# Kernel tuning notes

Measured on AMD Instinct MI355X. Metric: run time of the kernel, lower is better.

The kernel has to match this reference:

```python
import jax, jax.numpy as jnp
import numpy as np

N = 8192

def setup_inputs() -> dict:
    key = jax.random.key(0)
    adj = jax.random.uniform(key, (N, N), dtype=jnp.float32)
    return {"adj": adj}

def reference(adj) -> jnp.ndarray:
    # Symmetrize: adj + adj_T*(adj_T>adj) - adj*(adj_T>adj) == elementwise max(adj, adj_T)
    a = jnp.maximum(adj, adj.T)
    # Add self-loops
    a = a + jnp.eye(a.shape[0], dtype=a.dtype)
    # Degree normalization: D^-1/2 A D^-1/2 (diag matmuls == broadcast row/col scaling)
    rowsum = jnp.sum(a, axis=1)
    d_inv_sqrt = jnp.power(rowsum, -0.5)
    d_inv_sqrt = jnp.where(jnp.isinf(d_inv_sqrt), 0.0, d_inv_sqrt)
    return d_inv_sqrt[:, None] * a * d_inv_sqrt[None, :]
```

## Files before the change

kernel.cpp:

```cpp
#include <hip/hip_runtime.h>
#include <math.h>

#define NMAT 8192
#define GT   128
#define NPAIRS (GT * (GT + 1) / 2)

typedef float f4 __attribute__((ext_vector_type(4)));

__device__ __align__(16) float g_part[GT][NMAT];
__device__ __align__(16) float g_dvec[NMAT];

__device__ __forceinline__ int tri_off(int b) {
    return b * GT - ((b * (b - 1)) >> 1);
}

__device__ __forceinline__ void decode_pair(int p, int& bi, int& bj) {
    double dp = (double)p;
    double t = 2.0 * GT + 1.0;
    int b = (int)((t - sqrt(t * t - 8.0 * dp)) * 0.5);
    if (b < 0) b = 0;
    if (b > GT - 1) b = GT - 1;
    while (b + 1 < GT && tri_off(b + 1) <= p) ++b;
    while (b > 0 && tri_off(b) > p) --b;
    bi = b;
    bj = b + (p - tri_off(b));
}

__global__ __launch_bounds__(256) void calc_d() {
    int i = blockIdx.x * blockDim.x + threadIdx.x;
    if (i < NMAT) {
        float s = 1.0f;
        #pragma unroll 8
        for (int c = 0; c < GT; ++c) s += g_part[c][i];
        g_dvec[i] = (s > 0.0f) ? (float)(1.0 / sqrt((double)s)) : 0.0f;
    }
}

__global__ __launch_bounds__(256) void pass1_rowsum(const float* __restrict__ A) {
    __shared__ float Yl[64][65];
    __shared__ float colbuf[4][64];

    int bi, bj;
    decode_pair((int)blockIdx.x, bi, bj);

    const int tid   = threadIdx.x;
    const int l16   = tid & 15;
    const int g16   = tid >> 4;
    const int cbase = l16 * 4;
    const int lane  = tid & 63;
    const int w     = tid >> 6;

    const float* Ybase = A + (size_t)(bj * 64) * NMAT + bi * 64;
    const float* Xbase = A + (size_t)(bi * 64) * NMAT + bj * 64;

    f4 y[4], x[4];
    for (int k = 0; k < 4; ++k) {
        int q = k * 16 + g16;
        y[k] = *(const f4*)(Ybase + (size_t)q * NMAT + cbase);
    }
    for (int k = 0; k < 4; ++k) {
        int r = k * 16 + g16;
        x[k] = *(const f4*)(Xbase + (size_t)r * NMAT + cbase);
    }

    for (int k = 0; k < 4; ++k) {
        int q = k * 16 + g16;
        Yl[q][cbase + 0] = y[k].x;
        Yl[q][cbase + 1] = y[k].y;
        Yl[q][cbase + 2] = y[k].z;
        Yl[q][cbase + 3] = y[k].w;
    }
    __syncthreads();

    float cs0 = 0.f, cs1 = 0.f, cs2 = 0.f, cs3 = 0.f;

    for (int k = 0; k < 4; ++k) {
        int r = k * 16 + g16;
        float m0 = fmaxf(x[k].x, Yl[cbase + 0][r]);
        float m1 = fmaxf(x[k].y, Yl[cbase + 1][r]);
        float m2 = fmaxf(x[k].z, Yl[cbase + 2][r]);
        float m3 = fmaxf(x[k].w, Yl[cbase + 3][r]);
        cs0 += m0; cs1 += m1; cs2 += m2; cs3 += m3;
        float rt = (m0 + m1) + (m2 + m3);
        rt += __shfl_xor(rt, 1);
        rt += __shfl_xor(rt, 2);
        rt += __shfl_xor(rt, 4);
        rt += __shfl_xor(rt, 8);
        if (l16 == 0) g_part[bj][bi * 64 + r] = rt;
    }

    if (bi != bj) {
        cs0 += __shfl_xor(cs0, 16); cs0 += __shfl_xor(cs0, 32);
        cs1 += __shfl_xor(cs1, 16); cs1 += __shfl_xor(cs1, 32);
        cs2 += __shfl_xor(cs2, 16); cs2 += __shfl_xor(cs2, 32);
        cs3 += __shfl_xor(cs3, 16); cs3 += __shfl_xor(cs3, 32);
        if (lane < 16) {
            colbuf[w][lane * 4 + 0] = cs0;
            colbuf[w][lane * 4 + 1] = cs1;
            colbuf[w][lane * 4 + 2] = cs2;
            colbuf[w][lane * 4 + 3] = cs3;
        }
        __syncthreads();
        if (tid < 64) {
            float t = (colbuf[0][tid] + colbuf[1][tid]) +
                      (colbuf[2][tid] + colbuf[3][tid]);
            g_part[bi][bj * 64 + tid] = t;
        }
    }
}

__global__ __launch_bounds__(256) void pass2_scale(const float* __restrict__ A,
                                                   float* __restrict__ out) {
    __shared__ float Yl[64][65];

    int bi, bj;
    decode_pair(NPAIRS - 1 - (int)blockIdx.x, bi, bj);

    const int tid   = threadIdx.x;
    const int l16   = tid & 15;
    const int g16   = tid >> 4;
    const int cbase = l16 * 4;

    const float* Ybase = A + (size_t)(bj * 64) * NMAT + bi * 64;
    const float* Xbase = A + (size_t)(bi * 64) * NMAT + bj * 64;

    f4 y[4], x[4];
    for (int k = 0; k < 4; ++k) {
        int q = k * 16 + g16;
        y[k] = *(const f4*)(Ybase + (size_t)q * NMAT + cbase);
    }
    for (int k = 0; k < 4; ++k) {
        int r = k * 16 + g16;
        x[k] = *(const f4*)(Xbase + (size_t)r * NMAT + cbase);
    }

    for (int k = 0; k < 4; ++k) {
        int q = k * 16 + g16;
        Yl[q][cbase + 0] = y[k].x;
        Yl[q][cbase + 1] = y[k].y;
        Yl[q][cbase + 2] = y[k].z;
        Yl[q][cbase + 3] = y[k].w;
    }
    __syncthreads();

    const f4 dj = *(const f4*)(g_dvec + bj * 64 + cbase);
    const bool diag = (bi == bj);

    for (int k = 0; k < 4; ++k) {
        int r = k * 16 + g16;
        float di = g_dvec[bi * 64 + r];
        float m0 = fmaxf(x[k].x, Yl[cbase + 0][r]);
        float m1 = fmaxf(x[k].y, Yl[cbase + 1][r]);
        float m2 = fmaxf(x[k].z, Yl[cbase + 2][r]);
        float m3 = fmaxf(x[k].w, Yl[cbase + 3][r]);
        if (diag) {
            if (r == cbase + 0) m0 += 1.0f;
            if (r == cbase + 1) m1 += 1.0f;
            if (r == cbase + 2) m2 += 1.0f;
            if (r == cbase + 3) m3 += 1.0f;
        }
        f4 v;
        v.x = di * dj.x * m0;
        v.y = di * dj.y * m1;
        v.z = di * dj.z * m2;
        v.w = di * dj.w * m3;
        __builtin_nontemporal_store(v, (f4*)(out + (size_t)(bi * 64 + r) * NMAT + bj * 64 + cbase));
        Yl[cbase + 0][r] = v.x;
        Yl[cbase + 1][r] = v.y;
        Yl[cbase + 2][r] = v.z;
        Yl[cbase + 3][r] = v.w;
    }

    if (!diag) {
        __syncthreads();
        for (int k = 0; k < 4; ++k) {
            int q = k * 16 + g16;
            f4 v;
            v.x = Yl[q][cbase + 0];
            v.y = Yl[q][cbase + 1];
            v.z = Yl[q][cbase + 2];
            v.w = Yl[q][cbase + 3];
            __builtin_nontemporal_store(v, (f4*)(out + (size_t)(bj * 64 + q) * NMAT + bi * 64 + cbase));
        }
    }
}

extern "C" void kernel_launch(void* const* d_in, const int* in_sizes, int n_in,
                              void* d_out, int out_size, void* d_ws, size_t ws_size,
                              hipStream_t stream) {
    const float* A = (const float*)d_in[0];
    float* out     = (float*)d_out;

    pass1_rowsum<<<NPAIRS, 256, 0, stream>>>(A);
    calc_d<<<NMAT / 256, 256, 0, stream>>>();
    pass2_scale<<<NPAIRS, 256, 0, stream>>>(A, out);
}
```

Measured before the change: 489.4 us.

## Enlarge transpose tiles to 128x128 with XOR-swizzled shared memory

Doubles the symmetric tile size from 64 to 128, using 1024-thread blocks and half as many tile-row partials. Shared-memory bank conflicts are avoided with an XOR swizzle of the column index instead of padding. Diagonal tiles reuse the already-loaded block instead of loading the transposed copy a second time. Larger blocks with 64KB of shared memory each may limit how many blocks fit per CU and reduce latency hiding.

New measurement: 469.9 us. -4.0%, faster.

```diff
diff --git a/kernel.cpp b/kernel.cpp
--- a/kernel.cpp
+++ b/kernel.cpp
@@ -2,7 +2,8 @@
 #include <math.h>
 
 #define NMAT 8192
-#define GT   128
+#define TS   128
+#define GT   (NMAT / TS)
 #define NPAIRS (GT * (GT + 1) / 2)
 
 typedef float f4 __attribute__((ext_vector_type(4)));
@@ -36,123 +37,135 @@
     }
 }
 
-__global__ __launch_bounds__(256) void pass1_rowsum(const float* __restrict__ A) {
-    __shared__ float Yl[64][65];
-    __shared__ float colbuf[4][64];
+__global__ __launch_bounds__(1024) void pass1_rowsum(const float* __restrict__ A) {
+    __shared__ float Yl[TS][TS];
+    __shared__ float colbuf[16][TS];
 
     int bi, bj;
     decode_pair((int)blockIdx.x, bi, bj);
 
     const int tid   = threadIdx.x;
-    const int l16   = tid & 15;
-    const int g16   = tid >> 4;
-    const int cbase = l16 * 4;
-    const int lane  = tid & 63;
+    const int l32   = tid & 31;
+    const int g32   = tid >> 5;
+    const int cbase = l32 * 4;
     const int w     = tid >> 6;
-
-    const float* Ybase = A + (size_t)(bj * 64) * NMAT + bi * 64;
-    const float* Xbase = A + (size_t)(bi * 64) * NMAT + bj * 64;
-
-    f4 y[4], x[4];
-    for (int k = 0; k < 4; ++k) {
-        int q = k * 16 + g16;
-        y[k] = *(const f4*)(Ybase + (size_t)q * NMAT + cbase);
-    }
-    for (int k = 0; k < 4; ++k) {
-        int r = k * 16 + g16;
-        x[k] = *(const f4*)(Xbase + (size_t)r * NMAT + cbase);
-    }
-
-    for (int k = 0; k < 4; ++k) {
-        int q = k * 16 + g16;
-        Yl[q][cbase + 0] = y[k].x;
-        Yl[q][cbase + 1] = y[k].y;
-        Yl[q][cbase + 2] = y[k].z;
-        Yl[q][cbase + 3] = y[k].w;
+    const bool diag = (bi == bj);
+
+    const float* Xbase = A + (size_t)(bi * TS) * NMAT + bj * TS;
+    const float* Ybase = A + (size_t)(bj * TS) * NMAT + bi * TS;
+
+    f4 x[4], y[4];
+    #pragma unroll
+    for (int k = 0; k < 4; ++k)
+        x[k] = *(const f4*)(Xbase + (size_t)(k * 32 + g32) * NMAT + cbase);
+    if (!diag) {
+        #pragma unroll
+        for (int k = 0; k < 4; ++k)
+            y[k] = *(const f4*)(Ybase + (size_t)(k * 32 + g32) * NMAT + cbase);
+    }
+
+    #pragma unroll
+    for (int k = 0; k < 4; ++k) {
+        int r = k * 32 + g32;
+        f4 v = diag ? x[k] : y[k];
+        int s = (r >> 2) & 31;
+        Yl[r][(cbase + 0) ^ s] = v.x;
+        Yl[r][(cbase + 1) ^ s] = v.y;
+        Yl[r][(cbase + 2) ^ s] = v.z;
+        Yl[r][(cbase + 3) ^ s] = v.w;
     }
     __syncthreads();
 
     float cs0 = 0.f, cs1 = 0.f, cs2 = 0.f, cs3 = 0.f;
 
-    for (int k = 0; k < 4; ++k) {
-        int r = k * 16 + g16;
-        float m0 = fmaxf(x[k].x, Yl[cbase + 0][r]);
-        float m1 = fmaxf(x[k].y, Yl[cbase + 1][r]);
-        float m2 = fmaxf(x[k].z, Yl[cbase + 2][r]);
-        float m3 = fmaxf(x[k].w, Yl[cbase + 3][r]);
+    #pragma unroll
+    for (int k = 0; k < 4; ++k) {
+        int r  = k * 32 + g32;
+        int rs = r ^ l32;
+        float m0 = fmaxf(x[k].x, Yl[cbase + 0][rs]);
+        float m1 = fmaxf(x[k].y, Yl[cbase + 1][rs]);
+        float m2 = fmaxf(x[k].z, Yl[cbase + 2][rs]);
+        float m3 = fmaxf(x[k].w, Yl[cbase + 3][rs]);
         cs0 += m0; cs1 += m1; cs2 += m2; cs3 += m3;
         float rt = (m0 + m1) + (m2 + m3);
         rt += __shfl_xor(rt, 1);
         rt += __shfl_xor(rt, 2);
         rt += __shfl_xor(rt, 4);
         rt += __shfl_xor(rt, 8);
-        if (l16 == 0) g_part[bj][bi * 64 + r] = rt;
-    }
-
-    if (bi != bj) {
-        cs0 += __shfl_xor(cs0, 16); cs0 += __shfl_xor(cs0, 32);
-        cs1 += __shfl_xor(cs1, 16); cs1 += __shfl_xor(cs1, 32);
-        cs2 += __shfl_xor(cs2, 16); cs2 += __shfl_xor(cs2, 32);
-        cs3 += __shfl_xor(cs3, 16); cs3 += __shfl_xor(cs3, 32);
-        if (lane < 16) {
-            colbuf[w][lane * 4 + 0] = cs0;
-            colbuf[w][lane * 4 + 1] = cs1;
-            colbuf[w][lane * 4 + 2] = cs2;
-            colbuf[w][lane * 4 + 3] = cs3;
+        rt += __shfl_xor(rt, 16);
+        if (l32 == 0) g_part[bj][bi * TS + r] = rt;
+    }
+
+    if (!diag) {
+        cs0 += __shfl_xor(cs0, 32);
+        cs1 += __shfl_xor(cs1, 32);
+        cs2 += __shfl_xor(cs2, 32);
+        cs3 += __shfl_xor(cs3, 32);
+        if (!(tid & 32)) {
+            colbuf[w][cbase + 0] = cs0;
+            colbuf[w][cbase + 1] = cs1;
+            colbuf[w][cbase + 2] = cs2;
+            colbuf[w][cbase + 3] = cs3;
         }
         __syncthreads();
-        if (tid < 64) {
-            float t = (colbuf[0][tid] + colbuf[1][tid]) +
-                      (colbuf[2][tid] + colbuf[3][tid]);
-            g_part[bi][bj * 64 + tid] = t;
-        }
-    }
-}
-
-__global__ __launch_bounds__(256) void pass2_scale(const float* __restrict__ A,
-                                                   float* __restrict__ out) {
-    __shared__ float Yl[64][65];
+        if (tid < TS) {
+            float t = 0.f;
+            #pragma unroll
+            for (int v = 0; v < 16; ++v) t += colbuf[v][tid];
+            g_part[bi][bj * TS + tid] = t;
+        }
+    }
+}
+
+__global__ __launch_bounds__(1024) void pass2_scale(const float* __restrict__ A,
+                                                    float* __restrict__ out) {
+    __shared__ float Yl[TS][TS];
 
     int bi, bj;
     decode_pair(NPAIRS - 1 - (int)blockIdx.x, bi, bj);
 
     const int tid   = threadIdx.x;
-    const int l16   = tid & 15;
-    const int g16   = tid >> 4;
-    const int cbase = l16 * 4;
-
-    const float* Ybase = A + (size_t)(bj * 64) * NMAT + bi * 64;
-    const float* Xbase = A + (size_t)(bi * 64) * NMAT + bj * 64;
-
-    f4 y[4], x[4];
-    for (int k = 0; k < 4; ++k) {
-        int q = k * 16 + g16;
-        y[k] = *(const f4*)(Ybase + (size_t)q * NMAT + cbase);
-    }
-    for (int k = 0; k < 4; ++k) {
-        int r = k * 16 + g16;
-        x[k] = *(const f4*)(Xbase + (size_t)r * NMAT + cbase);
-    }
-
-    for (int k = 0; k < 4; ++k) {
-        int q = k * 16 + g16;
-        Yl[q][cbase + 0] = y[k].x;
-        Yl[q][cbase + 1] = y[k].y;
-        Yl[q][cbase + 2] = y[k].z;
-        Yl[q][cbase + 3] = y[k].w;
+    const int l32   = tid & 31;
+    const int g32   = tid >> 5;
+    const int cbase = l32 * 4;
+    const bool diag = (bi == bj);
+
+    const float* Xbase = A + (size_t)(bi * TS) * NMAT + bj * TS;
+    const float* Ybase = A + (size_t)(bj * TS) * NMAT + bi * TS;
+
+    f4 x[4], y[4];
+    #pragma unroll
+    for (int k = 0; k < 4; ++k)
+        x[k] = *(const f4*)(Xbase + (size_t)(k * 32 + g32) * NMAT + cbase);
+    if (!diag) {
+        #pragma unroll
+        for (int k = 0; k < 4; ++k)
+            y[k] = *(const f4*)(Ybase + (size_t)(k * 32 + g32) * NMAT + cbase);
+    }
+
+    #pragma unroll
+    for (int k = 0; k < 4; ++k) {
+        int r = k * 32 + g32;
+        f4 v = diag ? x[k] : y[k];
+        int s = (r >> 2) & 31;
+        Yl[r][(cbase + 0) ^ s] = v.x;
+        Yl[r][(cbase + 1) ^ s] = v.y;
+        Yl[r][(cbase + 2) ^ s] = v.z;
+        Yl[r][(cbase + 3) ^ s] = v.w;
     }
     __syncthreads();
 
-    const f4 dj = *(const f4*)(g_dvec + bj * 64 + cbase);
-    const bool diag = (bi == bj);
-
-    for (int k = 0; k < 4; ++k) {
-        int r = k * 16 + g16;
-        float di = g_dvec[bi * 64 + r];
-        float m0 = fmaxf(x[k].x, Yl[cbase + 0][r]);
-        float m1 = fmaxf(x[k].y, Yl[cbase + 1][r]);
-        float m2 = fmaxf(x[k].z, Yl[cbase + 2][r]);
-        float m3 = fmaxf(x[k].w, Yl[cbase + 3][r]);
+    const f4 dj = *(const f4*)(g_dvec + bj * TS + cbase);
+
+    #pragma unroll
+    for (int k = 0; k < 4; ++k) {
+        int r  = k * 32 + g32;
+        int rs = r ^ l32;
+        float di = g_dvec[bi * TS + r];
+        float m0 = fmaxf(x[k].x, Yl[cbase + 0][rs]);
+        float m1 = fmaxf(x[k].y, Yl[cbase + 1][rs]);
+        float m2 = fmaxf(x[k].z, Yl[cbase + 2][rs]);
+        float m3 = fmaxf(x[k].w, Yl[cbase + 3][rs]);
         if (diag) {
             if (r == cbase + 0) m0 += 1.0f;
             if (r == cbase + 1) m1 += 1.0f;
@@ -164,23 +177,25 @@
         v.y = di * dj.y * m1;
         v.z = di * dj.z * m2;
         v.w = di * dj.w * m3;
-        __builtin_nontemporal_store(v, (f4*)(out + (size_t)(bi * 64 + r) * NMAT + bj * 64 + cbase));
-        Yl[cbase + 0][r] = v.x;
-        Yl[cbase + 1][r] = v.y;
-        Yl[cbase + 2][r] = v.z;
-        Yl[cbase + 3][r] = v.w;
+        __builtin_nontemporal_store(v, (f4*)(out + (size_t)(bi * TS + r) * NMAT + bj * TS + cbase));
+        Yl[cbase + 0][rs] = v.x;
+        Yl[cbase + 1][rs] = v.y;
+        Yl[cbase + 2][rs] = v.z;
+        Yl[cbase + 3][rs] = v.w;
     }
 
     if (!diag) {
         __syncthreads();
+        #pragma unroll
         for (int k = 0; k < 4; ++k) {
-            int q = k * 16 + g16;
+            int q  = k * 32 + g32;
+            int sq = (q >> 2) & 31;
             f4 v;
-            v.x = Yl[q][cbase + 0];
-            v.y = Yl[q][cbase + 1];
-            v.z = Yl[q][cbase + 2];
-            v.w = Yl[q][cbase + 3];
-            __builtin_nontemporal_store(v, (f4*)(out + (size_t)(bj * 64 + q) * NMAT + bi * 64 + cbase));
+            v.x = Yl[q][(cbase + 0) ^ sq];
+            v.y = Yl[q][(cbase + 1) ^ sq];
+            v.z = Yl[q][(cbase + 2) ^ sq];
+            v.w = Yl[q][(cbase + 3) ^ sq];
+            __builtin_nontemporal_store(v, (f4*)(out + (size_t)(bj * TS + q) * NMAT + bi * TS + cbase));
         }
     }
 }
@@ -191,7 +206,7 @@
     const float* A = (const float*)d_in[0];
     float* out     = (float*)d_out;
 
-    pass1_rowsum<<<NPAIRS, 256, 0, stream>>>(A);
+    pass1_rowsum<<<NPAIRS, 1024, 0, stream>>>(A);
     calc_d<<<NMAT / 256, 256, 0, stream>>>();
-    pass2_scale<<<NPAIRS, 256, 0, stream>>>(A, out);
-}
+    pass2_scale<<<NPAIRS, 1024, 0, stream>>>(A, out);
+}
```
